# Performance work log

Hardware: AMD Instinct MI355X
Metric: run time of the kernel (lower is better)

The kernel has to match this reference:

```python
import jax, jax.numpy as jnp
import numpy as np

ITER = 50
HEADS = 8

def _ln(x, g, b, eps=1e-5):
    m = jnp.mean(x, -1, keepdims=True)
    v = jnp.var(x, -1, keepdims=True)
    return (x - m) * jax.lax.rsqrt(v + eps) * g + b

def _glu(x):
    a, b = jnp.split(x, 2, -1)
    return a * jax.nn.sigmoid(b)

def setup_inputs() -> dict:
    key = jax.random.key(0)
    ks = iter(jax.random.split(key, 48))
    B, D, E, M, H, O, NA, NO = 64, 2048, 512, 25, 32, 4096, 512, 512
    def nrm(shape, fan):
        return jax.random.normal(next(ks), shape, jnp.float32) / np.float32(np.sqrt(fan))
    return dict(
        x=jax.random.normal(next(ks), (B, 12, 8, 8), jnp.float32),
        kv_w=nrm((12, E), 12), kv_b=jnp.zeros(E), kv_ln_g=jnp.ones(E), kv_ln_b=jnp.zeros(E),
        q_w=nrm((NA, E), NA), q_b=jnp.zeros(E),
        wq=nrm((E, E), E), wk=nrm((E, E), E), wv=nrm((E, E), E), wo=nrm((E, E), E),
        bq=jnp.zeros(E), bk=jnp.zeros(E), bv=jnp.zeros(E), bo=jnp.zeros(E),
        syn_w=nrm((E + D, 2 * D), E + D), syn_b=jnp.zeros(2 * D),
        syn_ln_g=jnp.ones(D), syn_ln_b=jnp.zeros(D),
        nlm1_w=nrm((M, 2 * H, D), M), nlm1_b=jnp.zeros((D, 2 * H)),
        nlm2_w=nrm((H, 2, D), H), nlm2_b=jnp.zeros((D, 2)),
        start_activated_state=nrm((D,), D), start_trace=nrm((D, M), D + M),
        decay_action=jax.random.uniform(next(ks), (NA,)) * 0.5,
        decay_out=jax.random.uniform(next(ks), (NO,)) * 0.5,
        out_w=nrm((NO, O), NO), out_b=jnp.zeros(O),
        idx_a_left=jax.random.randint(next(ks), (NA,), 0, D, jnp.int32),
        idx_a_right=jax.random.randint(next(ks), (NA,), 0, D, jnp.int32),
        idx_o_left=jax.random.randint(next(ks), (NO,), 0, D, jnp.int32),
        idx_o_right=jax.random.randint(next(ks), (NO,), 0, D, jnp.int32),
    )

def reference(x, kv_w, kv_b, kv_ln_g, kv_ln_b, q_w, q_b, wq, wk, wv, wo, bq, bk, bv, bo,
              syn_w, syn_b, syn_ln_g, syn_ln_b, nlm1_w, nlm1_b, nlm2_w, nlm2_b,
              start_activated_state, start_trace, decay_action, decay_out, out_w, out_b,
              idx_a_left, idx_a_right, idx_o_left, idx_o_right):
    B = x.shape[0]
    D, M = start_trace.shape
    E = kv_w.shape[1]
    O = out_w.shape[1]
    Dh = E // HEADS
    # compute_features: backbone=none, pos=none -> flatten(2).transpose(1,2) then kv_proj
    feats = x.reshape(B, x.shape[1], -1).transpose(0, 2, 1)          # (B, 64, 12)
    kv = _ln(feats @ kv_w + kv_b, kv_ln_g, kv_ln_b)                  # (B, 64, E)
    kp = (kv @ wk + bk).reshape(B, -1, HEADS, Dh)                    # precompute K/V once
    vp = (kv @ wv + bv).reshape(B, -1, HEADS, Dh)
    r_a = jnp.exp(-jnp.clip(decay_action, 0.0, 15.0))
    r_o = jnp.exp(-jnp.clip(decay_out, 0.0, 15.0))
    trace0 = jnp.broadcast_to(start_trace, (B, D, M))
    act0 = jnp.broadcast_to(start_activated_state, (B, D))
    zA = jnp.zeros((B, decay_action.shape[0]))
    zO = jnp.zeros((B, decay_out.shape[0]))
    inv_sqrt_dh = np.float32(1.0 / np.sqrt(Dh))
    inv_log_o = np.float32(1.0 / np.log(O))

    def step(carry, _):
        trace, act, aA, bA, aO, bO = carry
        # action synchronisation (random-pairing: elementwise pair product, decayed)
        pw = act[:, idx_a_left] * act[:, idx_a_right]
        aA = r_a * aA + pw
        bA = r_a * bA + 1.0
        sync_a = aA * jax.lax.rsqrt(bA)
        # single-query MHA over the 64 board tokens
        q = sync_a @ q_w + q_b
        qh = (q @ wq + bq).reshape(B, HEADS, Dh)
        sc = jnp.einsum('bhd,bshd->bhs', qh, kp) * inv_sqrt_dh
        attn = jax.nn.softmax(sc, -1)
        o = jnp.einsum('bhs,bshd->bhd', attn, vp).reshape(B, E)
        attn_out = o @ wo + bo
        # synapse MLP (Linear -> GLU -> LayerNorm)
        pre = jnp.concatenate([attn_out, act], -1)
        state = _ln(_glu(pre @ syn_w + syn_b), syn_ln_g, syn_ln_b)   # (B, D)
        # shift memory trace and run per-neuron NLMs
        trace = jnp.concatenate([trace[:, :, 1:], state[:, :, None]], -1)
        h = _glu(jnp.einsum('bnm,mhn->bnh', trace, nlm1_w) + nlm1_b)
        act = _glu(jnp.einsum('bnm,mhn->bnh', h, nlm2_w) + nlm2_b)[..., 0]
        # output synchronisation + prediction + certainty
        pwo = act[:, idx_o_left] * act[:, idx_o_right]
        aO = r_o * aO + pwo
        bO = r_o * bO + 1.0
        sync_o = aO * jax.lax.rsqrt(bO)
        pred = sync_o @ out_w + out_b
        logp = jax.nn.log_softmax(pred, -1)
        ne = -jnp.sum(jnp.exp(logp) * logp, -1) * inv_log_o
        cert = jnp.stack([ne, 1.0 - ne], -1)
        return (trace, act, aA, bA, aO, bO), (pred, cert)

    _, (preds, certs) = jax.lax.scan(step, (trace0, act0, zA, zA, zO, zO), None, length=ITER)
    predictions = preds.transpose(1, 2, 0)   # (B, out_dims, iterations)
    certainties = certs.transpose(1, 2, 0)   # (B, 2, iterations)
    return predictions, certainties
```

## Files before the change

### kernel.cpp

```cpp
#include <hip/hip_runtime.h>
#include <math.h>

#define NB 64
#define ND 2048
#define NE 512
#define NM 25
#define NOUT 4096
#define NHEADS 8
#define NDH 64
#define NS 64
#define NITER 50
#define NKSYN 2560
#define PRED_TOTAL (NB * NOUT * NITER)

typedef unsigned short bf16_t;
typedef __attribute__((ext_vector_type(8))) short short8;
typedef __attribute__((ext_vector_type(4))) float f32x4;

__device__ __forceinline__ float sigm(float x) { return 1.f / (1.f + expf(-x)); }

__device__ __forceinline__ bf16_t f2bf(float f) {
    unsigned u = __float_as_uint(f);
    unsigned r = (u + 0x7FFFu + ((u >> 16) & 1u)) >> 16;
    return (bf16_t)r;
}
__device__ __forceinline__ float bf2f(bf16_t h) {
    return __uint_as_float(((unsigned)h) << 16);
}

__device__ __forceinline__ float wredsum(float v) {
#pragma unroll
    for (int o = 32; o; o >>= 1) v += __shfl_xor(v, o);
    return v;
}
__device__ __forceinline__ float wredmax(float v) {
#pragma unroll
    for (int o = 32; o; o >>= 1) v = fmaxf(v, __shfl_xor(v, o));
    return v;
}

template <int OP>
__device__ __forceinline__ float blockReduce(float v, float* red) {
    const int tid = threadIdx.x, lane = tid & 63, wid = tid >> 6;
    v = (OP == 0) ? wredsum(v) : wredmax(v);
    __syncthreads();
    if (lane == 0) red[wid] = v;
    __syncthreads();
    if (tid == 0) {
        const int nw = blockDim.x >> 6;
        float r = red[0];
        for (int w = 1; w < nw; ++w) r = (OP == 0) ? r + red[w] : fmaxf(r, red[w]);
        red[0] = r;
    }
    __syncthreads();
    return red[0];
}


__global__ __launch_bounds__(512) void k_fo(
        const float* __restrict__ actT, bf16_t* __restrict__ actB,
        float* __restrict__ aA, float* __restrict__ bA,
        const float* __restrict__ r_a,
        const int* __restrict__ ial, const int* __restrict__ iar,
        const bf16_t* __restrict__ W_qqb, const float* __restrict__ b_qq,
        const bf16_t* __restrict__ kvp,
        float* __restrict__ aO, float* __restrict__ bO,
        const float* __restrict__ r_o,
        const int* __restrict__ iol, const int* __restrict__ ior,
        const bf16_t* __restrict__ boutw, float* __restrict__ part_out,
        int doFront, int doOut, int it) {
    __shared__ float lds[8192];
    const int bid = blockIdx.x;
    const int t = threadIdx.x;
    const int lane = t & 63, wv = t >> 6;

    if (bid >= 256) {
        if (!doOut) return;
        const int itO = it - 1;
        const int srcO = itO & 1, dstO = srcO ^ 1;
        const int half = t >> 8, t2 = t & 255;
        const int unit = (bid - 256) * 2 + half;
        const int kp = unit >> 6, jt2 = unit & 63;
        float* sL = lds + half * 4096;
#pragma unroll
        for (int c = 0; c < 16; ++c) {
            const int idx = t2 + c * 256;
            const int il = idx >> 6, bb = idx & 63;
            const int i = kp * 64 + il;
            const float pl = actT[iol[i] * NB + bb];
            const float prr = actT[ior[i] * NB + bb];
            const float r = r_o[i];
            const float aN = r * aO[srcO * 32768 + i * NB + bb] + pl * prr;
            const float bN = r * bO[srcO * 32768 + i * NB + bb] + 1.f;
            if (jt2 == 0) {
                aO[dstO * 32768 + i * NB + bb] = aN;
                bO[dstO * 32768 + i * NB + bb] = bN;
            }
            sL[il * 64 + bb] = aN * rsqrtf(bN);
        }
        __syncthreads();
        const int bb = t2 & 63;
        const int j0 = jt2 * 64 + __builtin_amdgcn_readfirstlane((t2 >> 6) & 3) * 16;
        float acc[16];
#pragma unroll
        for (int q = 0; q < 16; ++q) acc[q] = 0.f;
#pragma unroll 4
        for (int k = 0; k < 64; ++k) {
            const float sv = sL[k * 64 + bb];
            const unsigned* wrow = (const unsigned*)(boutw + (size_t)(kp * 64 + k) * NOUT + j0);
#pragma unroll
            for (int q = 0; q < 8; ++q) {
                const unsigned u = wrow[q];
                const float w0 = __uint_as_float(u << 16);
                const float w1 = __uint_as_float(u & 0xffff0000u);
                acc[2 * q + 0] = fmaf(sv, w0, acc[2 * q + 0]);
                acc[2 * q + 1] = fmaf(sv, w1, acc[2 * q + 1]);
            }
        }
        float* dstp = part_out + ((size_t)(kp * NB + bb)) * NOUT + j0;
#pragma unroll
        for (int q = 0; q < 16; ++q) dstp[q] = acc[q];
        return;
    }

    if (!doFront) return;
    float* syncS = lds;
    float* partK = lds + 512;
    float* qhS = lds + 1024;
    float* attnS = lds + 1152;
    const int jt = bid >> 6, b = bid & 63;
    const int src = it & 1, dst = src ^ 1;
    {
        const int i = t;
        const float pl = actT[ial[i] * NB + b];
        const float prr = actT[iar[i] * NB + b];
        const float r = r_a[i];
        const float aN = r * aA[src * 32768 + b * NE + i] + pl * prr;
        const float bN = r * bA[src * 32768 + b * NE + i] + 1.f;
        if (jt == 0) {
            aA[dst * 32768 + b * NE + i] = aN;
            bA[dst * 32768 + b * NE + i] = bN;
        }
        syncS[i] = aN * rsqrtf(bN);
    }
    __syncthreads();
    {
        const int g = t >> 7, l = t & 127;
        const int j = jt * 128 + l;
        float acc = 0.f;
        const int kk0 = g * 128;
#pragma unroll 4
        for (int k = kk0; k < kk0 + 128; ++k)
            acc = fmaf(syncS[k], bf2f(W_qqb[k * NE + j]), acc);
        partK[g * 128 + l] = acc;
    }
    __syncthreads();
    if (t < 128) {
        qhS[t] = b_qq[jt * 128 + t] + partK[t] + partK[128 + t] + partK[256 + t] + partK[384 + t];
    }
    __syncthreads();
    if (wv < 2) {
        const int h = jt * 2 + wv, s = lane;
        const bf16_t* kpp = kvp + ((size_t)(b * NS + s) * 1024 + h * NDH);
        float sc = 0.f;
#pragma unroll 8
        for (int d = 0; d < NDH; ++d) sc = fmaf(qhS[wv * 64 + d], bf2f(kpp[d]), sc);
        sc *= 0.125f;
        const float mxv = wredmax(sc);
        const float ev = expf(sc - mxv);
        const float sm = wredsum(ev);
        attnS[wv * 64 + s] = ev / sm;
    }
    __syncthreads();
    if (wv < 2) {
        const int h = jt * 2 + wv, d = lane;
        const bf16_t* vpp = kvp + ((size_t)(b * NS) * 1024 + NE + h * NDH + d);
        float o = 0.f;
#pragma unroll 8
        for (int s2 = 0; s2 < NS; ++s2) o = fmaf(attnS[wv * 64 + s2], bf2f(vpp[(size_t)s2 * 1024]), o);
        actB[(size_t)b * NKSYN + h * NDH + d] = f2bf(o);
    }
}

__global__ __launch_bounds__(256) void k_gf(
        const bf16_t* __restrict__ actB, const bf16_t* __restrict__ bpack,
        float* __restrict__ part_syn,
        const float* __restrict__ part_out, const float* __restrict__ out_b,
        float* __restrict__ out, float* __restrict__ predTemp,
        int doGemm, int doFinal, int tt, int tmode) {
    __shared__ float red[8];
    const int bid = blockIdx.x;
    const int t = threadIdx.x;
    if (bid < 512) {
        if (!doGemm) return;
        const int kp = bid >> 6, jt = bid & 63;
        const int l = t & 63;
        const int wv = t >> 6;
        const int b0 = wv * 16;
        const int row = b0 + (l & 15);
        const int kgrp = l >> 4;
        f32x4 acc[4];
#pragma unroll
        for (int js = 0; js < 4; ++js) acc[js] = (f32x4){0.f, 0.f, 0.f, 0.f};
        const int ks0 = kp * 10;
#pragma unroll 2
        for (int ks = 0; ks < 10; ++ks) {
            const int kk = (ks0 + ks) * 32;
            const short8 av = *(const short8*)(actB + (size_t)row * NKSYN + kk + kgrp * 8);
#pragma unroll
            for (int js = 0; js < 4; ++js) {
                const short8 bv = *(const short8*)(bpack +
                    ((((size_t)(jt * 4 + js)) * 80 + ks0 + ks) * 64 + l) * 8);
                acc[js] = __builtin_amdgcn_mfma_f32_16x16x32_bf16(av, bv, acc[js], 0, 0, 0);
            }
        }
#pragma unroll
        for (int js = 0; js < 4; ++js) {
#pragma unroll
            for (int r = 0; r < 4; ++r) {
                const int b = b0 + kgrp * 4 + r;
                const int j = jt * 64 + js * 16 + (l & 15);
                part_syn[((size_t)(kp * NB + b)) * NOUT + j] = acc[js][r];
            }
        }
    } else {
        if (!doFinal) return;
        const int b = bid - 512;
        float pr[16];
        float lmax = -1e30f;
#pragma unroll
        for (int c = 0; c < 16; ++c) {
            const int j = t + c * 256;
            float v = out_b[j];
#pragma unroll
            for (int kp = 0; kp < 8; ++kp) v += part_out[((size_t)(kp * NB + b)) * NOUT + j];
            pr[c] = v;
            lmax = fmaxf(lmax, v);
        }
        const float mx = blockReduce<1>(lmax, red);
        float ls = 0.f;
#pragma unroll
        for (int c = 0; c < 16; ++c) ls += expf(pr[c] - mx);
        const float se = blockReduce<0>(ls, red);
        const float logZ = mx + logf(se);
        float le = 0.f;
#pragma unroll
        for (int c = 0; c < 16; ++c) { const float lp = pr[c] - logZ; le += expf(lp) * lp; }
        const float ent = blockReduce<0>(le, red);
        const float ne = -ent * 0.12022458674074694f;
        if (tmode) {
#pragma unroll
            for (int c = 0; c < 16; ++c)
                predTemp[((size_t)b * NITER + tt) * NOUT + t + c * 256] = pr[c];
        } else {
#pragma unroll
            for (int c = 0; c < 16; ++c) {
                const int j = t + c * 256;
                out[((size_t)b * NOUT + j) * NITER + tt] = pr[c];
            }
        }
        if (t == 0) {
            out[PRED_TOTAL + b * 100 + tt] = ne;
            out[PRED_TOTAL + b * 100 + 50 + tt] = 1.f - ne;
        }
    }
}

__global__ __launch_bounds__(512) void k_glu(const float* __restrict__ part,
                                             const float* __restrict__ sbe,
                                             float* __restrict__ trace2,
                                             float* __restrict__ statsPart, int pos) {
    __shared__ float red[8];
    const int b = blockIdx.x >> 2, q = blockIdx.x & 3;
    const int t = threadIdx.x;
    const int n = q * 512 + t;
    float ya = sbe[n], yb = sbe[n + ND];
#pragma unroll
    for (int kp = 0; kp < 8; ++kp) {
        ya += part[((size_t)(kp * NB + b)) * NOUT + n];
        yb += part[((size_t)(kp * NB + b)) * NOUT + n + ND];
    }
    const float g = ya * sigm(yb);
    trace2[((size_t)pos * ND + n) * NB + b] = g;
    const float s = blockReduce<0>(g, red);
    const float ss = blockReduce<0>(g * g, red);
    if (t == 0) {
        statsPart[(blockIdx.x) * 2 + 0] = s;
        statsPart[(blockIdx.x) * 2 + 1] = ss;
    }
}

__global__ __launch_bounds__(256, 2) void k_nlm(float* __restrict__ trace2,
                                                const bf16_t* __restrict__ bw1t,
                                                const float* __restrict__ b1,
                                                const float* __restrict__ w2t,
                                                const float* __restrict__ b2,
                                                const float* __restrict__ statsPart,
                                                const float* __restrict__ ln_g,
                                                const float* __restrict__ ln_b,
                                                float* __restrict__ actT,
                                                bf16_t* __restrict__ actB, int pos) {
    __shared__ float tileA[4][64];
    const int b = threadIdx.x & 63;
    const int wvu = __builtin_amdgcn_readfirstlane(threadIdx.x >> 6);
    const int n = blockIdx.x * 4 + wvu;
    float ssum = 0.f, ssq = 0.f;
#pragma unroll
    for (int q = 0; q < 4; ++q) {
        ssum += statsPart[(b * 4 + q) * 2 + 0];
        ssq  += statsPart[(b * 4 + q) * 2 + 1];
    }
    const float mean = ssum * (1.f / ND);
    const float rs = rsqrtf(ssq * (1.f / ND) - mean * mean + 1e-5f);

    const float* brow = b1 + n * 64;
    float acc[64];
#pragma unroll
    for (int q = 0; q < 64; ++q) acc[q] = brow[q];
    int phys = (pos + 1 < NM) ? pos + 1 : 0;
    float tr = trace2[((size_t)phys * ND + n) * NB + b];
#pragma unroll 1
    for (int m = 0; m < NM - 1; ++m) {
        const int physN = (phys + 1 < NM) ? phys + 1 : 0;
        float trn = 0.f;
        if (m + 1 < NM - 1) trn = trace2[((size_t)physN * ND + n) * NB + b];
        const unsigned* wrow = (const unsigned*)(bw1t + ((size_t)n * NM + m) * 64);
#pragma unroll
        for (int q = 0; q < 32; ++q) {
            const unsigned u = wrow[q];
            const float w0 = __uint_as_float(u << 16);
            const float w1 = __uint_as_float(u & 0xffff0000u);
            acc[2 * q + 0] = fmaf(tr, w0, acc[2 * q + 0]);
            acc[2 * q + 1] = fmaf(tr, w1, acc[2 * q + 1]);
        }
        tr = trn; phys = physN;
    }
    {
        const float raw = trace2[((size_t)pos * ND + n) * NB + b];
        const float trNew = (raw - mean) * rs * ln_g[n] + ln_b[n];
        trace2[((size_t)pos * ND + n) * NB + b] = trNew;
        const unsigned* wrow = (const unsigned*)(bw1t + ((size_t)n * NM + (NM - 1)) * 64);
#pragma unroll
        for (int q = 0; q < 32; ++q) {
            const unsigned u = wrow[q];
            const float w0 = __uint_as_float(u << 16);
            const float w1 = __uint_as_float(u & 0xffff0000u);
            acc[2 * q + 0] = fmaf(trNew, w0, acc[2 * q + 0]);
            acc[2 * q + 1] = fmaf(trNew, w1, acc[2 * q + 1]);
        }
    }
    const float* w2r = w2t + n * 64;
    float z0 = b2[n * 2 + 0], z1 = b2[n * 2 + 1];
#pragma unroll
    for (int i = 0; i < 32; ++i) {
        const float hv = acc[i] * sigm(acc[32 + i]);
        z0 = fmaf(hv, w2r[i], z0);
        z1 = fmaf(hv, w2r[32 + i], z1);
    }
    const float val = z0 * sigm(z1);
    actT[n * NB + b] = val;
    tileA[wvu][b] = val;
    __syncthreads();
    const int bb = threadIdx.x >> 2, nn = threadIdx.x & 3;
    actB[(size_t)bb * NKSYN + NE + blockIdx.x * 4 + nn] = f2bf(tileA[nn][bb]);
}


__global__ __launch_bounds__(256) void k_p0(const float* __restrict__ dec_a,
                                            const float* __restrict__ dec_o,
                                            const float* __restrict__ q_b,
                                            const float* __restrict__ wq,
                                            const float* __restrict__ bq,
                                            float* __restrict__ r_a, float* __restrict__ r_o,
                                            float* __restrict__ b_qq) {
    const int t = threadIdx.x;
    if (blockIdx.x == 0) {
        for (int i = t; i < NE; i += 256) {
            r_a[i] = expf(-fminf(fmaxf(dec_a[i], 0.f), 15.f));
            r_o[i] = expf(-fminf(fmaxf(dec_o[i], 0.f), 15.f));
        }
        return;
    }
    __shared__ float partial[4][64];
    const int c = (blockIdx.x - 1) * 64 + (t & 63);
    const int kg = t >> 6;
    float acc = 0.f;
#pragma unroll 4
    for (int k = kg * 128; k < kg * 128 + 128; ++k)
        acc = fmaf(q_b[k], wq[k * NE + c], acc);
    partial[kg][t & 63] = acc;
    __syncthreads();
    if (t < 64) {
        const int cc = (blockIdx.x - 1) * 64 + t;
        b_qq[cc] = bq[cc] + partial[0][t] + partial[1][t] + partial[2][t] + partial[3][t];
    }
}

__global__ __launch_bounds__(256) void k_packB(const float* __restrict__ src,
                                               int ld, int nbj, int ksgs,
                                               bf16_t* __restrict__ dst) {
    __shared__ float tile[32][65];
    const int ksg = blockIdx.x / nbj;
    const int bj = blockIdx.x % nbj;
    const int k0 = ksg * 32, j0 = bj * 64;
    for (int i = threadIdx.x; i < 2048; i += 256) {
        const int kk = i >> 6, jj = i & 63;
        tile[kk][jj] = src[(size_t)(k0 + kk) * ld + j0 + jj];
    }
    __syncthreads();
    for (int i = threadIdx.x; i < 2048; i += 256) {
        const int j16 = i >> 9;
        const int ii = i & 511;
        const int e = ii & 7, l = ii >> 3;
        const int kk = (l >> 4) * 8 + e;
        const int jj = j16 * 16 + (l & 15);
        dst[(((size_t)(bj * 4 + j16) * ksgs + ksg) * 64) * 8 + ii] = f2bf(tile[kk][jj]);
    }
}

__global__ __launch_bounds__(256, 2) void k_woSynM(const bf16_t* __restrict__ bwo,
                                                   const bf16_t* __restrict__ synw0p,
                                                   float* __restrict__ woSyn) {
    const int mt = blockIdx.x >> 6, nt = blockIdx.x & 63;
    const int l = threadIdx.x & 63;
    const int w = threadIdx.x >> 6;
    const int row0 = mt * 64 + w * 16;
    const int row = row0 + (l & 15);
    const int kgrp = l >> 4;
    f32x4 acc[4];
#pragma unroll
    for (int js = 0; js < 4; ++js) acc[js] = (f32x4){0.f, 0.f, 0.f, 0.f};
#pragma unroll 2
    for (int ks = 0; ks < 16; ++ks) {
        const short8 av = *(const short8*)(bwo + (size_t)row * NE + ks * 32 + kgrp * 8);
#pragma unroll
        for (int js = 0; js < 4; ++js) {
            const short8 bv8 = *(const short8*)(synw0p +
                ((((size_t)(nt * 4 + js)) * 16 + ks) * 64 + l) * 8);
            acc[js] = __builtin_amdgcn_mfma_f32_16x16x32_bf16(av, bv8, acc[js], 0, 0, 0);
        }
    }
#pragma unroll
    for (int js = 0; js < 4; ++js) {
#pragma unroll
        for (int r = 0; r < 4; ++r) {
            const int e = row0 + kgrp * 4 + r;
            const int c = nt * 64 + js * 16 + (l & 15);
            woSyn[(size_t)e * NOUT + c] = acc[js][r];
        }
    }
}

__global__ __launch_bounds__(256, 2) void k_wqqM(const bf16_t* __restrict__ bqw,
                                                 const bf16_t* __restrict__ wqp,
                                                 bf16_t* __restrict__ W_qqb) {
    const int mt = blockIdx.x >> 3, nt = blockIdx.x & 7;
    const int l = threadIdx.x & 63;
    const int w = threadIdx.x >> 6;
    const int row0 = mt * 64 + w * 16;
    const int row = row0 + (l & 15);
    const int kgrp = l >> 4;
    f32x4 acc[4];
#pragma unroll
    for (int js = 0; js < 4; ++js) acc[js] = (f32x4){0.f, 0.f, 0.f, 0.f};
#pragma unroll 2
    for (int ks = 0; ks < 16; ++ks) {
        const short8 av = *(const short8*)(bqw + (size_t)row * NE + ks * 32 + kgrp * 8);
#pragma unroll
        for (int js = 0; js < 4; ++js) {
            const short8 bv8 = *(const short8*)(wqp +
                ((((size_t)(nt * 4 + js)) * 16 + ks) * 64 + l) * 8);
            acc[js] = __builtin_amdgcn_mfma_f32_16x16x32_bf16(av, bv8, acc[js], 0, 0, 0);
        }
    }
#pragma unroll
    for (int js = 0; js < 4; ++js) {
#pragma unroll
        for (int r = 0; r < 4; ++r) {
            const int e = row0 + kgrp * 4 + r;
            const int c = nt * 64 + js * 16 + (l & 15);
            W_qqb[(size_t)e * NE + c] = f2bf(acc[js][r]);
        }
    }
}

__global__ __launch_bounds__(256) void k_sbe(const float* __restrict__ syn_b,
                                             const float* __restrict__ bo,
                                             const float* __restrict__ syn_w,
                                             float* __restrict__ sbe) {
    __shared__ float partial[4][64];
    const int c = blockIdx.x * 64 + (threadIdx.x & 63);
    const int kg = threadIdx.x >> 6;
    float acc = 0.f;
#pragma unroll 4
    for (int jp = kg * 128; jp < kg * 128 + 128; ++jp)
        acc = fmaf(bo[jp], syn_w[(size_t)jp * NOUT + c], acc);
    partial[kg][threadIdx.x & 63] = acc;
    __syncthreads();
    if (threadIdx.x < 64) {
        const int cc = blockIdx.x * 64 + threadIdx.x;
        sbe[cc] = syn_b[cc] + partial[0][threadIdx.x] + partial[1][threadIdx.x]
                + partial[2][threadIdx.x] + partial[3][threadIdx.x];
    }
}

__global__ __launch_bounds__(256) void k_cvt(const float* __restrict__ s,
                                             bf16_t* __restrict__ d) {
    const size_t i = (size_t)blockIdx.x * 256 + threadIdx.x;
    d[i] = f2bf(s[i]);
}

__global__ __launch_bounds__(256) void k_bpack(const float* __restrict__ woSyn,
                                               const float* __restrict__ syn_w,
                                               bf16_t* __restrict__ bpack) {
    __shared__ float tile[32][65];
    const int ksg = blockIdx.x >> 6;
    const int bj = blockIdx.x & 63;
    const int k0 = ksg * 32, j0 = bj * 64;
    for (int i = threadIdx.x; i < 2048; i += 256) {
        const int kk = i >> 6, jj = i & 63;
        const int k = k0 + kk;
        tile[kk][jj] = (k < NE) ? woSyn[(size_t)k * NOUT + j0 + jj]
                                : syn_w[(size_t)k * NOUT + j0 + jj];
    }
    __syncthreads();
    for (int i = threadIdx.x; i < 2048; i += 256) {
        const int j16 = i >> 9;
        const int ii = i & 511;
        const int e = ii & 7, l = ii >> 3;
        const int kk = (l >> 4) * 8 + e;
        const int jj = j16 * 16 + (l & 15);
        bpack[(((size_t)(bj * 4 + j16) * 80 + ksg) * 64) * 8 + ii] = f2bf(tile[kk][jj]);
    }
}

__global__ __launch_bounds__(256) void k_wkvpack(const float* __restrict__ wk,
                                                 const float* __restrict__ wv,
                                                 bf16_t* __restrict__ wkvpack) {
    __shared__ float tile[32][65];
    const int ksg = blockIdx.x >> 4;
    const int bj = blockIdx.x & 15;
    const int k0 = ksg * 32, j0 = bj * 64;
    for (int i = threadIdx.x; i < 2048; i += 256) {
        const int kk = i >> 6, jj = i & 63;
        const int k = k0 + kk, j = j0 + jj;
        tile[kk][jj] = (j < NE) ? wk[(size_t)k * NE + j] : wv[(size_t)k * NE + (j - NE)];
    }
    __syncthreads();
    for (int i = threadIdx.x; i < 2048; i += 256) {
        const int j16 = i >> 9;
        const int ii = i & 511;
        const int e = ii & 7, l = ii >> 3;
        const int kk = (l >> 4) * 8 + e;
        const int jj = j16 * 16 + (l & 15);
        wkvpack[(((size_t)(bj * 4 + j16) * 16 + ksg) * 64) * 8 + ii] = f2bf(tile[kk][jj]);
    }
}

__global__ __launch_bounds__(256) void k_init_trace2(const float* __restrict__ st,
                                                     float* __restrict__ trace2) {
    const int idx = blockIdx.x * 256 + threadIdx.x;
    const int n = (idx >> 6) & (ND - 1);
    const int m = idx >> 17;
    trace2[idx] = st[n * NM + m];
}

#define INIT_TOTAL (NB * ND + 8 * NB * NE)
__global__ __launch_bounds__(256) void k_init_state(const float* __restrict__ sa,
                                                    float* __restrict__ actT,
                                                    bf16_t* __restrict__ actB,
                                                    float* __restrict__ zeroBase) {
    const int idx = blockIdx.x * 256 + threadIdx.x;
    if (idx >= INIT_TOTAL) return;
    if (idx < NB * ND) {
        const int b = idx & 63, n = idx >> 6;
        actT[n * NB + b] = sa[n];
        actB[(size_t)b * NKSYN + NE + n] = f2bf(sa[n]);
    } else {
        zeroBase[idx - NB * ND] = 0.f;
    }
}

__global__ __launch_bounds__(512) void k_p1a(const float* __restrict__ x,
                                             const float* __restrict__ kv_w,
                                             const float* __restrict__ kv_b,
                                             const float* __restrict__ ln_g,
                                             const float* __restrict__ ln_b,
                                             bf16_t* __restrict__ kvnB) {
    __shared__ float kvT[NE][17];
    __shared__ float mS[16], rS[16];
    const int b = blockIdx.x >> 2, s0 = (blockIdx.x & 3) * 16;
    const int t = threadIdx.x;
    const int lane = t & 63, wvi = t >> 6;

    {
        float w[12];
#pragma unroll
        for (int c = 0; c < 12; ++c) w[c] = kv_w[c * NE + t];
        const float kb = kv_b[t];
#pragma unroll
        for (int tok = 0; tok < 16; ++tok) {
            float acc = kb;
#pragma unroll
            for (int c = 0; c < 12; ++c)
                acc = fmaf(x[b * 768 + c * 64 + s0 + tok], w[c], acc);
            kvT[t][tok] = acc;
        }
    }
    __syncthreads();
#pragma unroll
    for (int q = 0; q < 2; ++q) {
        const int tok = wvi * 2 + q;
        float s = 0.f, ss = 0.f;
#pragma unroll
        for (int i = 0; i < 8; ++i) {
            const float v = kvT[lane + 64 * i][tok];
            s += v; ss = fmaf(v, v, ss);
        }
        s = wredsum(s); ss = wredsum(ss);
        if (lane == 0) {
            const float mean = s * (1.f / NE);
            mS[tok] = mean;
            rS[tok] = rsqrtf(ss * (1.f / NE) - mean * mean + 1e-5f);
        }
    }
    __syncthreads();
    {
        const float g = ln_g[t], bb2 = ln_b[t];
#pragma unroll
        for (int tok = 0; tok < 16; ++tok) {
            const float kvn = (kvT[t][tok] - mS[tok]) * rS[tok] * g + bb2;
            kvnB[(size_t)(b * 64 + s0 + tok) * NE + t] = f2bf(kvn);
        }
    }
}

__global__ __launch_bounds__(256, 2) void k_p1b(const bf16_t* __restrict__ kvnB,
                                                const bf16_t* __restrict__ wkvpack,
                                                const float* __restrict__ bk,
                                                const float* __restrict__ bv,
                                                bf16_t* __restrict__ kvp) {
    const int mt = blockIdx.x >> 4, nt = blockIdx.x & 15;
    const int l = threadIdx.x & 63;
    const int wv = threadIdx.x >> 6;
    const int row0 = mt * 64 + wv * 16;
    const int row = row0 + (l & 15);
    const int kgrp = l >> 4;
    f32x4 acc[4];
#pragma unroll
    for (int js = 0; js < 4; ++js) acc[js] = (f32x4){0.f, 0.f, 0.f, 0.f};
#pragma unroll 2
    for (int ks = 0; ks < 16; ++ks) {
        const short8 av = *(const short8*)(kvnB + (size_t)row * NE + ks * 32 + kgrp * 8);
#pragma unroll
        for (int js = 0; js < 4; ++js) {
            const short8 bv8 = *(const short8*)(wkvpack +
                ((((size_t)(nt * 4 + js)) * 16 + ks) * 64 + l) * 8);
            acc[js] = __builtin_amdgcn_mfma_f32_16x16x32_bf16(av, bv8, acc[js], 0, 0, 0);
        }
    }
#pragma unroll
    for (int js = 0; js < 4; ++js) {
#pragma unroll
        for (int r = 0; r < 4; ++r) {
            const int tok = row0 + kgrp * 4 + r;
            const int j = nt * 64 + js * 16 + (l & 15);
            const float bias = (j < NE) ? bk[j] : bv[j - NE];
            kvp[(size_t)tok * 1024 + j] = f2bf(acc[js][r] + bias);
        }
    }
}

__global__ __launch_bounds__(256) void k_w1t(const float* __restrict__ w1,
                                             bf16_t* __restrict__ bw1t) {
    __shared__ float tile[64][65];
    const int m = blockIdx.x >> 5, n0 = (blockIdx.x & 31) << 6;
    for (int i = threadIdx.x; i < 4096; i += 256) {
        const int hh = i >> 6, nn = i & 63;
        tile[hh][nn] = w1[(size_t)(m * 64 + hh) * ND + n0 + nn];
    }
    __syncthreads();
    for (int i = threadIdx.x; i < 4096; i += 256) {
        const int nn = i >> 6, hh = i & 63;
        bw1t[((size_t)(n0 + nn) * NM + m) * 64 + hh] = f2bf(tile[hh][nn]);
    }
}

__global__ __launch_bounds__(256) void k_w2t(const float* __restrict__ w2,
                                             float* __restrict__ w2t) {
    const int idx = blockIdx.x * 256 + threadIdx.x;
    const int i = idx & 31;
    const int c = (idx >> 5) & 1;
    const int n = idx >> 6;
    w2t[idx] = w2[(size_t)(i * 2 + c) * ND + n];
}

__global__ __launch_bounds__(256) void k_transpose(const float* __restrict__ predTemp,
                                                   float* __restrict__ out) {
    __shared__ float tile[NS * NITER];
    const int b = blockIdx.x >> 6;
    const int j0 = (blockIdx.x & 63) * 64;
    for (int i = threadIdx.x; i < 3200; i += 256) {
        const int tt = i >> 6, jj = i & 63;
        tile[jj * NITER + tt] = predTemp[((size_t)b * NITER + tt) * NOUT + j0 + jj];
    }
    __syncthreads();
    float* dst = out + ((size_t)b * NOUT + j0) * NITER;
    for (int i = threadIdx.x; i < 3200; i += 256) dst[i] = tile[i];
}

extern "C" void kernel_launch(void* const* d_in, const int* in_sizes, int n_in,
                              void* d_out, int out_size, void* d_ws, size_t ws_size,
                              hipStream_t stream) {
    const float* x        = (const float*)d_in[0];
    const float* kv_w     = (const float*)d_in[1];
    const float* kv_b     = (const float*)d_in[2];
    const float* kv_ln_g  = (const float*)d_in[3];
    const float* kv_ln_b  = (const float*)d_in[4];
    const float* q_w      = (const float*)d_in[5];
    const float* q_b      = (const float*)d_in[6];
    const float* wq       = (const float*)d_in[7];
    const float* wk       = (const float*)d_in[8];
    const float* wv       = (const float*)d_in[9];
    const float* wo       = (const float*)d_in[10];
    const float* bq       = (const float*)d_in[11];
    const float* bk       = (const float*)d_in[12];
    const float* bv       = (const float*)d_in[13];
    const float* bo       = (const float*)d_in[14];
    const float* syn_w    = (const float*)d_in[15];
    const float* syn_b    = (const float*)d_in[16];
    const float* syn_ln_g = (const float*)d_in[17];
    const float* syn_ln_b = (const float*)d_in[18];
    const float* nlm1_w   = (const float*)d_in[19];
    const float* nlm1_b   = (const float*)d_in[20];
    const float* nlm2_w   = (const float*)d_in[21];
    const float* nlm2_b   = (const float*)d_in[22];
    const float* start_a  = (const float*)d_in[23];
    const float* start_tr = (const float*)d_in[24];
    const float* dec_a    = (const float*)d_in[25];
    const float* dec_o    = (const float*)d_in[26];
    const float* out_w    = (const float*)d_in[27];
    const float* out_b    = (const float*)d_in[28];
    const int* ial        = (const int*)d_in[29];
    const int* iar        = (const int*)d_in[30];
    const int* iol        = (const int*)d_in[31];
    const int* ior        = (const int*)d_in[32];
    float* out = (float*)d_out;

    float* ws = (float*)d_ws;
    size_t off = 0;
    auto alloc = [&](size_t n) { float* p = ws + off; off += n; return p; };
    float* actT      = alloc((size_t)ND * NB);
    bf16_t* actB     = (bf16_t*)alloc((size_t)NB * NKSYN / 2);
    bf16_t* kvnB     = (bf16_t*)alloc((size_t)NB * NS * NE / 2);
    bf16_t* kvp      = (bf16_t*)alloc((size_t)NB * NS * 1024 / 2);
    bf16_t* wkvpack  = (bf16_t*)alloc((size_t)NE * 1024 / 2);
    bf16_t* W_qqb    = (bf16_t*)alloc((size_t)NE * NE / 2);
    bf16_t* boutw    = (bf16_t*)alloc((size_t)NE * NOUT / 2);
    bf16_t* bwo      = (bf16_t*)alloc((size_t)NE * NE / 2);
    bf16_t* bqw      = (bf16_t*)alloc((size_t)NE * NE / 2);
    bf16_t* synw0p   = (bf16_t*)alloc((size_t)NE * NOUT / 2);
    bf16_t* wqp      = (bf16_t*)alloc((size_t)NE * NE / 2);
    float* woSyn     = alloc((size_t)NE * NOUT);
    bf16_t* bpack    = (bf16_t*)alloc((size_t)NKSYN * NOUT / 2);
    float* sbe       = alloc(NOUT);
    float* b_qq      = alloc(NE);
    float* r_a       = alloc(NE);
    float* r_o       = alloc(NE);
    float* statsPart = alloc(512);
    float* aA        = alloc((size_t)2 * NB * NE);
    float* bA        = alloc((size_t)2 * NB * NE);
    float* aO        = alloc((size_t)2 * NB * NE);
    float* bO        = alloc((size_t)2 * NB * NE);
    float* trace2    = alloc((size_t)NM * ND * NB);
    float* part_syn  = alloc((size_t)8 * NB * NOUT);
    float* part_out  = alloc((size_t)8 * NB * NOUT);
    bf16_t* bw1t     = (bf16_t*)alloc((size_t)ND * NM * 64 / 2);
    float* w2t       = alloc((size_t)ND * 64);
    int tmode = 0;
    float* predTemp = nullptr;
    if ((off + (size_t)PRED_TOTAL) * sizeof(float) <= ws_size) {
        predTemp = alloc((size_t)PRED_TOTAL);
        tmode = 1;
    }

    k_p0<<<9, 256, 0, stream>>>(dec_a, dec_o, q_b, wq, bq, r_a, r_o, b_qq);
    k_cvt<<<(NE * NE) / 256, 256, 0, stream>>>(wo, bwo);
    k_cvt<<<(NE * NE) / 256, 256, 0, stream>>>(q_w, bqw);
    k_packB<<<16 * 64, 256, 0, stream>>>(syn_w, NOUT, 64, 16, synw0p);
    k_packB<<<16 * 8, 256, 0, stream>>>(wq, NE, 8, 16, wqp);
    k_woSynM<<<512, 256, 0, stream>>>(bwo, synw0p, woSyn);
    k_wqqM<<<64, 256, 0, stream>>>(bqw, wqp, W_qqb);
    k_sbe<<<64, 256, 0, stream>>>(syn_b, bo, syn_w, sbe);
    k_bpack<<<5120, 256, 0, stream>>>(woSyn, syn_w, bpack);
    k_wkvpack<<<256, 256, 0, stream>>>(wk, wv, wkvpack);
    k_cvt<<<(NE * NOUT) / 256, 256, 0, stream>>>(out_w, boutw);
    k_init_trace2<<<(NM * ND * NB) / 256, 256, 0, stream>>>(start_tr, trace2);
    k_init_state<<<(INIT_TOTAL + 255) / 256, 256, 0, stream>>>(start_a, actT, actB, aA);
    k_p1a<<<256, 512, 0, stream>>>(x, kv_w, kv_b, kv_ln_g, kv_ln_b, kvnB);
    k_p1b<<<1024, 256, 0, stream>>>(kvnB, wkvpack, bk, bv, kvp);
    k_w1t<<<800, 256, 0, stream>>>(nlm1_w, bw1t);
    k_w2t<<<(ND * 64) / 256, 256, 0, stream>>>(nlm2_w, w2t);

    for (int t = 0; t < NITER; ++t) {
        k_fo<<<512, 512, 0, stream>>>(actT, actB, aA, bA, r_a, ial, iar, W_qqb, b_qq,
                                      kvp, aO, bO, r_o, iol, ior, boutw, part_out,
                                      1, (t > 0) ? 1 : 0, t);
        k_gf<<<576, 256, 0, stream>>>(actB, bpack, part_syn, part_out, out_b, out, predTemp,
                                      1, (t > 0) ? 1 : 0, t - 1, tmode);
        k_glu<<<256, 512, 0, stream>>>(part_syn, sbe, trace2, statsPart, t % NM);
        k_nlm<<<512, 256, 0, stream>>>(trace2, bw1t, nlm1_b, w2t, nlm2_b, statsPart,
                                       syn_ln_g, syn_ln_b, actT, actB, t % NM);
    }
    k_fo<<<512, 512, 0, stream>>>(actT, actB, aA, bA, r_a, ial, iar, W_qqb, b_qq,
                                  kvp, aO, bO, r_o, iol, ior, boutw, part_out,
                                  0, 1, NITER);
    k_gf<<<576, 256, 0, stream>>>(actB, bpack, part_syn, part_out, out_b, out, predTemp,
                                  0, 1, NITER - 1, tmode);
    if (tmode) k_transpose<<<NB * 64, 256, 0, stream>>>(predTemp, out);
}
```

Measured before the change: 3.484 ms.

## Fuse synapse GEMM split-K reduction with GLU and LayerNorm stats

```diff
diff --git a/kernel.cpp b/kernel.cpp
--- a/kernel.cpp
+++ b/kernel.cpp
@@ -182,50 +182,89 @@
     }
 }
 
-__global__ __launch_bounds__(256) void k_gf(
-        const bf16_t* __restrict__ actB, const bf16_t* __restrict__ bpack,
-        float* __restrict__ part_syn,
+__global__ __launch_bounds__(256) void k_gfg(
+        const bf16_t* __restrict__ actB, const bf16_t* __restrict__ bpack2,
+        const float* __restrict__ sbe,
+        float* __restrict__ trace2, float* __restrict__ statsPart,
         const float* __restrict__ part_out, const float* __restrict__ out_b,
         float* __restrict__ out, float* __restrict__ predTemp,
-        int doGemm, int doFinal, int tt, int tmode) {
+        int doGemm, int doFinal, int tt, int tmode, int pos) {
+    __shared__ float red4[4][4][64][4];
     __shared__ float red[8];
     const int bid = blockIdx.x;
     const int t = threadIdx.x;
-    if (bid < 512) {
+    if (bid < 256) {
         if (!doGemm) return;
-        const int kp = bid >> 6, jt = bid & 63;
-        const int l = t & 63;
-        const int wv = t >> 6;
-        const int b0 = wv * 16;
-        const int row = b0 + (l & 15);
+        const int tilei = bid;
+        const int l = t & 63, w = t >> 6;
         const int kgrp = l >> 4;
         f32x4 acc[4];
 #pragma unroll
-        for (int js = 0; js < 4; ++js) acc[js] = (f32x4){0.f, 0.f, 0.f, 0.f};
-        const int ks0 = kp * 10;
+        for (int rg = 0; rg < 4; ++rg) acc[rg] = (f32x4){0.f, 0.f, 0.f, 0.f};
+        const int ks0 = w * 20;
 #pragma unroll 2
-        for (int ks = 0; ks < 10; ++ks) {
-            const int kk = (ks0 + ks) * 32;
-            const short8 av = *(const short8*)(actB + (size_t)row * NKSYN + kk + kgrp * 8);
-#pragma unroll
-            for (int js = 0; js < 4; ++js) {
-                const short8 bv = *(const short8*)(bpack +
-                    ((((size_t)(jt * 4 + js)) * 80 + ks0 + ks) * 64 + l) * 8);
-                acc[js] = __builtin_amdgcn_mfma_f32_16x16x32_bf16(av, bv, acc[js], 0, 0, 0);
+        for (int ks = 0; ks < 20; ++ks) {
+            const short8 bv = *(const short8*)(bpack2 +
+                (((size_t)tilei * 80 + ks0 + ks) * 64 + l) * 8);
+            const int kk = (ks0 + ks) * 32 + kgrp * 8;
+#pragma unroll
+            for (int rg = 0; rg < 4; ++rg) {
+                const short8 av = *(const short8*)(actB + (size_t)(rg * 16 + (l & 15)) * NKSYN + kk);
+                acc[rg] = __builtin_amdgcn_mfma_f32_16x16x32_bf16(av, bv, acc[rg], 0, 0, 0);
             }
         }
 #pragma unroll
-        for (int js = 0; js < 4; ++js) {
+        for (int rg = 0; rg < 4; ++rg)
+#pragma unroll
+            for (int r = 0; r < 4; ++r) red4[w][rg][l][r] = acc[rg][r];
+        __syncthreads();
+        const int ct = t & 15, g = t >> 4;
+        const int rg = g >> 2, kg = g & 3;
+        const int lsrc = kg * 16 + ct;
+        const int colg = tilei * 8 + (ct & 7) + ((ct >= 8) ? ND : 0);
+        const float bias = sbe[colg];
+        float val[4];
+#pragma unroll
+        for (int r = 0; r < 4; ++r)
+            val[r] = red4[0][rg][lsrc][r] + red4[1][rg][lsrc][r]
+                   + red4[2][rg][lsrc][r] + red4[3][rg][lsrc][r] + bias;
+        float gv[4];
+#pragma unroll
+        for (int r = 0; r < 4; ++r) {
+            const float yb = __shfl_xor(val[r], 8);
+            gv[r] = val[r] * sigm(yb);
+        }
+        float s[4], q[4];
+#pragma unroll
+        for (int r = 0; r < 4; ++r) {
+            const float gr = (ct < 8) ? gv[r] : 0.f;
+            s[r] = gr; q[r] = gr * gr;
+        }
+        if (ct < 8) {
+            const int n = tilei * 8 + ct;
+#pragma unroll
+            for (int r = 0; r < 4; ++r)
+                trace2[((size_t)pos * ND + n) * NB + (g * 4 + r)] = gv[r];
+        }
+#pragma unroll
+        for (int o = 1; o < 8; o <<= 1) {
 #pragma unroll
             for (int r = 0; r < 4; ++r) {
-                const int b = b0 + kgrp * 4 + r;
-                const int j = jt * 64 + js * 16 + (l & 15);
-                part_syn[((size_t)(kp * NB + b)) * NOUT + j] = acc[js][r];
+                s[r] += __shfl_xor(s[r], o);
+                q[r] += __shfl_xor(q[r], o);
+            }
+        }
+        if (ct == 0) {
+#pragma unroll
+            for (int r = 0; r < 4; ++r) {
+                const int bb = g * 4 + r;
+                statsPart[((size_t)tilei * NB + bb) * 2 + 0] = s[r];
+                statsPart[((size_t)tilei * NB + bb) * 2 + 1] = q[r];
             }
         }
     } else {
         if (!doFinal) return;
-        const int b = bid - 512;
+        const int b = bid - 256;
         float pr[16];
         float lmax = -1e30f;
 #pragma unroll
@@ -263,30 +302,6 @@
             out[PRED_TOTAL + b * 100 + tt] = ne;
             out[PRED_TOTAL + b * 100 + 50 + tt] = 1.f - ne;
         }
-    }
-}
-
-__global__ __launch_bounds__(512) void k_glu(const float* __restrict__ part,
-                                             const float* __restrict__ sbe,
-                                             float* __restrict__ trace2,
-                                             float* __restrict__ statsPart, int pos) {
-    __shared__ float red[8];
-    const int b = blockIdx.x >> 2, q = blockIdx.x & 3;
-    const int t = threadIdx.x;
-    const int n = q * 512 + t;
-    float ya = sbe[n], yb = sbe[n + ND];
-#pragma unroll
-    for (int kp = 0; kp < 8; ++kp) {
-        ya += part[((size_t)(kp * NB + b)) * NOUT + n];
-        yb += part[((size_t)(kp * NB + b)) * NOUT + n + ND];
-    }
-    const float g = ya * sigm(yb);
-    trace2[((size_t)pos * ND + n) * NB + b] = g;
-    const float s = blockReduce<0>(g, red);
-    const float ss = blockReduce<0>(g * g, red);
-    if (t == 0) {
-        statsPart[(blockIdx.x) * 2 + 0] = s;
-        statsPart[(blockIdx.x) * 2 + 1] = ss;
     }
 }
 
@@ -301,15 +316,23 @@
                                                 float* __restrict__ actT,
                                                 bf16_t* __restrict__ actB, int pos) {
     __shared__ float tileA[4][64];
+    __shared__ float sred[2][4][64];
     const int b = threadIdx.x & 63;
     const int wvu = __builtin_amdgcn_readfirstlane(threadIdx.x >> 6);
     const int n = blockIdx.x * 4 + wvu;
-    float ssum = 0.f, ssq = 0.f;
-#pragma unroll
-    for (int q = 0; q < 4; ++q) {
-        ssum += statsPart[(b * 4 + q) * 2 + 0];
-        ssq  += statsPart[(b * 4 + q) * 2 + 1];
-    }
+    {
+        float ps = 0.f, pq = 0.f;
+#pragma unroll 8
+        for (int t2 = wvu * 64; t2 < wvu * 64 + 64; ++t2) {
+            ps += statsPart[((size_t)t2 * NB + b) * 2 + 0];
+            pq += statsPart[((size_t)t2 * NB + b) * 2 + 1];
+        }
+        sred[0][wvu][b] = ps;
+        sred[1][wvu][b] = pq;
+    }
+    __syncthreads();
+    const float ssum = sred[0][0][b] + sred[0][1][b] + sred[0][2][b] + sred[0][3][b];
+    const float ssq  = sred[1][0][b] + sred[1][1][b] + sred[1][2][b] + sred[1][3][b];
     const float mean = ssum * (1.f / ND);
     const float rs = rsqrtf(ssq * (1.f / ND) - mean * mean + 1e-5f);
 
@@ -510,27 +533,29 @@
     d[i] = f2bf(s[i]);
 }
 
-__global__ __launch_bounds__(256) void k_bpack(const float* __restrict__ woSyn,
-                                               const float* __restrict__ syn_w,
-                                               bf16_t* __restrict__ bpack) {
-    __shared__ float tile[32][65];
-    const int ksg = blockIdx.x >> 6;
-    const int bj = blockIdx.x & 63;
-    const int k0 = ksg * 32, j0 = bj * 64;
-    for (int i = threadIdx.x; i < 2048; i += 256) {
-        const int kk = i >> 6, jj = i & 63;
+__global__ __launch_bounds__(256) void k_bpack2(const float* __restrict__ woSyn,
+                                                const float* __restrict__ syn_w,
+                                                bf16_t* __restrict__ bpack2) {
+    __shared__ float tile[32][33];
+    const int ksg = blockIdx.x >> 7;
+    const int u = blockIdx.x & 127;
+    const int k0 = ksg * 32;
+    for (int i = threadIdx.x; i < 1024; i += 256) {
+        const int kk = i >> 5, jj = i & 31;
         const int k = k0 + kk;
-        tile[kk][jj] = (k < NE) ? woSyn[(size_t)k * NOUT + j0 + jj]
-                                : syn_w[(size_t)k * NOUT + j0 + jj];
-    }
-    __syncthreads();
-    for (int i = threadIdx.x; i < 2048; i += 256) {
-        const int j16 = i >> 9;
+        const int col = (jj < 16) ? (u * 16 + jj) : (ND + u * 16 + (jj - 16));
+        tile[kk][jj] = (k < NE) ? woSyn[(size_t)k * NOUT + col]
+                                : syn_w[(size_t)k * NOUT + col];
+    }
+    __syncthreads();
+    for (int i = threadIdx.x; i < 1024; i += 256) {
+        const int t2 = i >> 9;
         const int ii = i & 511;
         const int e = ii & 7, l = ii >> 3;
         const int kk = (l >> 4) * 8 + e;
-        const int jj = j16 * 16 + (l & 15);
-        bpack[(((size_t)(bj * 4 + j16) * 80 + ksg) * 64) * 8 + ii] = f2bf(tile[kk][jj]);
+        const int ci = l & 15;
+        const int jj = ci + ((ci >= 8) ? 8 : 0) + t2 * 8;
+        bpack2[(((size_t)(u * 2 + t2) * 80 + ksg) * 64) * 8 + ii] = f2bf(tile[kk][jj]);
     }
 }
 
@@ -592,7 +617,6 @@
     const int b = blockIdx.x >> 2, s0 = (blockIdx.x & 3) * 16;
     const int t = threadIdx.x;
     const int lane = t & 63, wvi = t >> 6;
-
     {
         float w[12];
 #pragma unroll
@@ -762,18 +786,17 @@
     bf16_t* synw0p   = (bf16_t*)alloc((size_t)NE * NOUT / 2);
     bf16_t* wqp      = (bf16_t*)alloc((size_t)NE * NE / 2);
     float* woSyn     = alloc((size_t)NE * NOUT);
-    bf16_t* bpack    = (bf16_t*)alloc((size_t)NKSYN * NOUT / 2);
+    bf16_t* bpack2   = (bf16_t*)alloc((size_t)NKSYN * NOUT / 2);
     float* sbe       = alloc(NOUT);
     float* b_qq      = alloc(NE);
     float* r_a       = alloc(NE);
     float* r_o       = alloc(NE);
-    float* statsPart = alloc(512);
+    float* statsPart = alloc((size_t)256 * NB * 2);
     float* aA        = alloc((size_t)2 * NB * NE);
     float* bA        = alloc((size_t)2 * NB * NE);
     float* aO        = alloc((size_t)2 * NB * NE);
     float* bO        = alloc((size_t)2 * NB * NE);
     float* trace2    = alloc((size_t)NM * ND * NB);
-    float* part_syn  = alloc((size_t)8 * NB * NOUT);
     float* part_out  = alloc((size_t)8 * NB * NOUT);
     bf16_t* bw1t     = (bf16_t*)alloc((size_t)ND * NM * 64 / 2);
     float* w2t       = alloc((size_t)ND * 64);
@@ -792,7 +815,7 @@
     k_woSynM<<<512, 256, 0, stream>>>(bwo, synw0p, woSyn);
     k_wqqM<<<64, 256, 0, stream>>>(bqw, wqp, W_qqb);
     k_sbe<<<64, 256, 0, stream>>>(syn_b, bo, syn_w, sbe);
-    k_bpack<<<5120, 256, 0, stream>>>(woSyn, syn_w, bpack);
+    k_bpack2<<<80 * 128, 256, 0, stream>>>(woSyn, syn_w, bpack2);
     k_wkvpack<<<256, 256, 0, stream>>>(wk, wv, wkvpack);
     k_cvt<<<(NE * NOUT) / 256, 256, 0, stream>>>(out_w, boutw);
     k_init_trace2<<<(NM * ND * NB) / 256, 256, 0, stream>>>(start_tr, trace2);
@@ -806,16 +829,17 @@
         k_fo<<<512, 512, 0, stream>>>(actT, actB, aA, bA, r_a, ial, iar, W_qqb, b_qq,
                                       kvp, aO, bO, r_o, iol, ior, boutw, part_out,
                                       1, (t > 0) ? 1 : 0, t);
-        k_gf<<<576, 256, 0, stream>>>(actB, bpack, part_syn, part_out, out_b, out, predTemp,
-                                      1, (t > 0) ? 1 : 0, t - 1, tmode);
-        k_glu<<<256, 512, 0, stream>>>(part_syn, sbe, trace2, statsPart, t % NM);
+        k_gfg<<<320, 256, 0, stream>>>(actB, bpack2, sbe, trace2, statsPart,
+                                       part_out, out_b, out, predTemp,
+                                       1, (t > 0) ? 1 : 0, t - 1, tmode, t % NM);
         k_nlm<<<512, 256, 0, stream>>>(trace2, bw1t, nlm1_b, w2t, nlm2_b, statsPart,
                                        syn_ln_g, syn_ln_b, actT, actB, t % NM);
     }
     k_fo<<<512, 512, 0, stream>>>(actT, actB, aA, bA, r_a, ial, iar, W_qqb, b_qq,
                                   kvp, aO, bO, r_o, iol, ior, boutw, part_out,
                                   0, 1, NITER);
-    k_gf<<<576, 256, 0, stream>>>(actB, bpack, part_syn, part_out, out_b, out, predTemp,
-                                  0, 1, NITER - 1, tmode);
+    k_gfg<<<320, 256, 0, stream>>>(actB, bpack2, sbe, trace2, statsPart,
+                                   part_out, out_b, out, predTemp,
+                                   0, 1, NITER - 1, tmode, 0);
     if (tmode) k_transpose<<<NB * 64, 256, 0, stream>>>(predTemp, out);
 }
```

Result: slower. 4.251 ms (+22.0%).
